# Kernel optimization log

Hardware: AMD Instinct MI355X
Metric: run time of the kernel (lower is better)

## Reference

```python
import jax, jax.numpy as jnp
import numpy as np

N_NODES = 100000
N_EDGES = 1600000
IN_C = 64
HID_C = 2 * IN_C  # 128
OUT_C = 64


def setup_inputs() -> dict:
    key = jax.random.key(0)
    k1, k2, k3, k4 = jax.random.split(key, 4)
    x = jax.random.normal(k1, (N_NODES, IN_C), dtype=jnp.float32)
    edge_index = jax.random.randint(k2, (2, N_EDGES), 0, N_NODES, dtype=jnp.int64)
    # Glorot-ish scaled weights
    W3 = jax.random.normal(k3, (IN_C, HID_C), dtype=jnp.float32) / np.sqrt(IN_C)
    b3 = jnp.zeros((HID_C,), dtype=jnp.float32)
    W4 = jax.random.normal(k4, (HID_C, OUT_C), dtype=jnp.float32) / np.sqrt(HID_C)
    b4 = jnp.zeros((OUT_C,), dtype=jnp.float32)
    return {"x": x, "edge_index": edge_index, "W3": W3, "b3": b3, "W4": W4, "b4": b4}


def _gcn_conv(x, src, dst, norm, W, b, n_nodes):
    # linear transform first (PyG GCNConv: lin then propagate), then
    # degree-normalized gather-scatter aggregation, then bias.
    h = x @ W                              # [N, C_out]
    msg = h[src] * norm[:, None]           # [E+N, C_out] gathered messages
    out = jax.ops.segment_sum(msg, dst, num_segments=n_nodes)
    return out + b


def reference(x, edge_index, W3, b3, W4, b4):
    n_nodes = x.shape[0]
    # add self-loops (PyG GCNConv default add_self_loops=True)
    loops = jnp.arange(n_nodes, dtype=edge_index.dtype)
    src = jnp.concatenate([edge_index[0], loops])  # [E+N]
    dst = jnp.concatenate([edge_index[1], loops])  # [E+N]
    # symmetric normalization: deg over target column incl. self-loops
    deg = jax.ops.segment_sum(jnp.ones(dst.shape, dtype=x.dtype), dst, num_segments=n_nodes)
    dinv = jnp.where(deg > 0, jax.lax.rsqrt(deg), jnp.zeros_like(deg))
    norm = dinv[src] * dinv[dst]                   # [E+N]
    h = jax.nn.relu(_gcn_conv(x, src, dst, norm, W3, b3, n_nodes))
    return _gcn_conv(h, src, dst, norm, W4, b4, n_nodes)
```

## Files before the change

kernel.cpp:

```cpp
#include <hip/hip_runtime.h>
#include <hip/hip_bf16.h>
#include <hip/hip_fp16.h>


constexpr int IN_C  = 64;
constexpr int HID_C = 128;
constexpr int OUT_C = 64;
constexpr int BSHIFT = 9;
constexpr int BW     = 1 << BSHIFT;
constexpr int TILE   = 4096;
constexpr int FCAP   = 16384;

typedef _Float16 f16x8 __attribute__((ext_vector_type(8)));
typedef float    f32x4 __attribute__((ext_vector_type(4)));

union FragU { uint4 u; f16x8 h; _Float16 q[8]; };

__device__ __forceinline__ f32x4 mfma16(f16x8 a, f16x8 b, f32x4 c) {
    return __builtin_amdgcn_mfma_f32_16x16x32_f16(a, b, c, 0, 0, 0);
}

__device__ __forceinline__ float2 up2(unsigned u) {
    __half2 h = *reinterpret_cast<__half2*>(&u);
    return __half22float2(h);
}
__device__ __forceinline__ unsigned pk2(float a, float b) {
    __half2 h = __float22half2_rn(make_float2(a, b));
    return *reinterpret_cast<unsigned*>(&h);
}

__global__ __launch_bounds__(256) void zero_small_kernel(int* __restrict__ p, int m)
{
    int i = blockIdx.x * 256 + threadIdx.x;
    if (i < m) p[i] = 0;
}

__global__ __launch_bounds__(256) void wfrag_kernel(
    const float* __restrict__ W3, const float* __restrict__ W4,
    uint4* __restrict__ w3f, uint4* __restrict__ w4f)
{
    const int idx = blockIdx.x * 256 + threadIdx.x;
    const int l = idx & 63, cl = l & 15, ch = l >> 4;
    if (idx < 2048) {
        const int fi = idx >> 6;
        const int h = fi & 1, s = (fi >> 1) & 1, c = fi >> 2;
        const int k0 = s * 32 + ch * 8, col = c * 16 + cl;
        FragU f;
        #pragma unroll
        for (int i = 0; i < 8; ++i) {
            float x = W3[(k0 + i) * HID_C + col];
            _Float16 hi = (_Float16)x;
            f.q[i] = h ? (_Float16)(x - (float)hi) : hi;
        }
        w3f[fi * 64 + l] = f.u;
    } else if (idx < 3072) {
        const int fi = (idx - 2048) >> 6;
        const int s = fi & 3, c = fi >> 2;
        const int k0 = s * 32 + ch * 8, col = c * 16 + cl;
        FragU f;
        #pragma unroll
        for (int i = 0; i < 8; ++i)
            f.q[i] = (_Float16)W4[(k0 + i) * OUT_C + col];
        w4f[fi * 64 + l] = f.u;
    }
}

__global__ __launch_bounds__(256) void bhist_kernel(
    const int* __restrict__ dst, int* __restrict__ bcnt, int E, int nbkt)
{
    __shared__ int h[256];
    h[threadIdx.x] = 0;
    __syncthreads();
    const int stride = gridDim.x * 256;
    for (int e = blockIdx.x * 256 + threadIdx.x; e < E; e += stride) {
        int d = __builtin_nontemporal_load(&dst[e]);
        atomicAdd(&h[d >> BSHIFT], 1);
    }
    __syncthreads();
    if (threadIdx.x < nbkt && h[threadIdx.x] != 0)
        atomicAdd(&bcnt[threadIdx.x], h[threadIdx.x]);
}

__global__ __launch_bounds__(256) void bscan_kernel(
    const int* __restrict__ bcnt, int* __restrict__ bbase,
    int* __restrict__ bcur, int nbkt)
{
    __shared__ int s[256];
    int v = (threadIdx.x < nbkt) ? bcnt[threadIdx.x] : 0;
    s[threadIdx.x] = v;
    __syncthreads();
    for (int off = 1; off < 256; off <<= 1) {
        int t = (threadIdx.x >= off) ? s[threadIdx.x - off] : 0;
        __syncthreads();
        s[threadIdx.x] += t;
        __syncthreads();
    }
    if (threadIdx.x < nbkt) {
        int ex = s[threadIdx.x] - v;
        bbase[threadIdx.x] = ex;
        bcur[threadIdx.x]  = ex;
        if (threadIdx.x == nbkt - 1) bbase[nbkt] = s[threadIdx.x];
    }
}

__global__ __launch_bounds__(256) void bin_kernel(
    const int* __restrict__ src, const int* __restrict__ dst,
    int* __restrict__ bcur, unsigned* __restrict__ ebuf, int E, int nbkt)
{
    __shared__ unsigned stageS[TILE];
    __shared__ unsigned char stageB[TILE];
    __shared__ int lcnt[256], lofs[256], lpos[256], gbase[256], s[256];
    const int base = blockIdx.x * TILE;
    const int cnt_mine = min(TILE, E - base);
    const int t = threadIdx.x;
    lcnt[t] = 0;
    __syncthreads();
    unsigned w[16]; int p[16];
    #pragma unroll
    for (int k = 0; k < 16; ++k) {
        int jo = t + k * 256;
        if (jo < cnt_mine) {
            int sv = __builtin_nontemporal_load(&src[base + jo]);
            int dv = __builtin_nontemporal_load(&dst[base + jo]);
            p[k] = dv >> BSHIFT;
            w[k] = ((unsigned)sv << BSHIFT) | (unsigned)(dv & (BW - 1));
            atomicAdd(&lcnt[p[k]], 1);
        } else p[k] = -1;
    }
    __syncthreads();
    int v = lcnt[t];
    s[t] = v;
    __syncthreads();
    for (int off = 1; off < 256; off <<= 1) {
        int u = (t >= off) ? s[t - off] : 0;
        __syncthreads();
        s[t] += u;
        __syncthreads();
    }
    lofs[t] = s[t] - v;
    lpos[t] = s[t] - v;
    if (t < nbkt && v != 0) gbase[t] = atomicAdd(&bcur[t], v);
    __syncthreads();
    #pragma unroll
    for (int k = 0; k < 16; ++k) {
        if (p[k] >= 0) {
            int pos = atomicAdd(&lpos[p[k]], 1);
            stageS[pos] = w[k];
            stageB[pos] = (unsigned char)p[k];
        }
    }
    __syncthreads();
    for (int j = t; j < cnt_mine; j += 256) {
        int b = stageB[j];
        ebuf[gbase[b] + (j - lofs[b])] = stageS[j];
    }
}

__global__ __launch_bounds__(256) void bucket_kernel(
    const unsigned* __restrict__ ebuf, const int* __restrict__ bbase,
    int* __restrict__ row_start, float* __restrict__ dinv,
    int* __restrict__ sorted_src, int n, int E, int nbkt)
{
    __shared__ int lcnt[BW];
    __shared__ int lcur[BW];
    __shared__ int s[256];
    __shared__ int lsrc[FCAP];
    const int b   = blockIdx.x;
    const int lo  = b << BSHIFT;
    const int hi  = min(lo + BW, n);
    const int nn  = hi - lo;
    const int beg = bbase[b], end = bbase[b + 1];
    const int cnt = end - beg;
    const int t   = threadIdx.x;
    for (int i = t; i < nn; i += 256) lcnt[i] = 0;
    __syncthreads();
    for (int j = beg + t; j < end; j += 256)
        atomicAdd(&lcnt[ebuf[j] & (BW - 1)], 1);
    __syncthreads();
    int a0 = (2 * t     < nn) ? lcnt[2 * t]     : 0;
    int a1 = (2 * t + 1 < nn) ? lcnt[2 * t + 1] : 0;
    int tsum = a0 + a1;
    s[t] = tsum;
    __syncthreads();
    for (int off = 1; off < 256; off <<= 1) {
        int v = (t >= off) ? s[t - off] : 0;
        __syncthreads();
        s[t] += v;
        __syncthreads();
    }
    int texcl = s[t] - tsum;
    if (2 * t < nn) {
        lcur[2 * t] = texcl;
        row_start[lo + 2 * t] = beg + texcl;
        dinv[lo + 2 * t] = rsqrtf((float)a0 + 1.0f);
    }
    if (2 * t + 1 < nn) {
        lcur[2 * t + 1] = texcl + a0;
        row_start[lo + 2 * t + 1] = beg + texcl + a0;
        dinv[lo + 2 * t + 1] = rsqrtf((float)a1 + 1.0f);
    }
    if (t == 0 && b == nbkt - 1) row_start[n] = E;
    __syncthreads();
    if (cnt <= FCAP) {
        for (int j = beg + t; j < end; j += 256) {
            unsigned w = ebuf[j];
            int pos = atomicAdd(&lcur[w & (BW - 1)], 1);
            lsrc[pos] = (int)(w >> BSHIFT);
        }
        __syncthreads();
        for (int j = t; j < cnt; j += 256)
            sorted_src[beg + j] = lsrc[j];
    } else {
        for (int j = beg + t; j < end; j += 256) {
            unsigned w = ebuf[j];
            int pos = atomicAdd(&lcur[w & (BW - 1)], 1);
            sorted_src[beg + pos] = (int)(w >> BSHIFT);
        }
    }
}

__global__ __launch_bounds__(256) void cvt_scaled_kernel(
    const float2* __restrict__ in, const float* __restrict__ dinv,
    unsigned* __restrict__ outw, int nw)
{
    int i = blockIdx.x * 256 + threadIdx.x;
    if (i < nw) {
        float2 v = in[i];
        float dv = dinv[i >> 5];
        outw[i] = pk2(v.x * dv, v.y * dv);
    }
}

template <bool OUT_F16, bool ADD_BIAS>
__global__ __launch_bounds__(256) void agg_f16_kernel(
    const unsigned* __restrict__ feat, const int* __restrict__ row_start,
    const int* __restrict__ sorted_src, const float* __restrict__ dinv,
    const float* __restrict__ bias, void* __restrict__ outp, int n)
{
    const int g  = threadIdx.x >> 3;
    const int gl = threadIdx.x & 7;
    const int d  = blockIdx.x * 32 + g;
    if (d >= n) return;
    const float di = dinv[d];
    const uint4* f4 = (const uint4*)feat;

    float a0x, a0y, a1x, a1y, a2x, a2y, a3x, a3y;
    {
        uint4 u = f4[(size_t)d * 8 + gl];
        float2 f0 = up2(u.x), f1 = up2(u.y), f2 = up2(u.z), f3 = up2(u.w);
        a0x = f0.x; a0y = f0.y; a1x = f1.x; a1y = f1.y;
        a2x = f2.x; a2y = f2.y; a3x = f3.x; a3y = f3.y;
    }

#define ACC(U) do { \
        float2 f0_ = up2((U).x), f1_ = up2((U).y), f2_ = up2((U).z), f3_ = up2((U).w); \
        a0x += f0_.x; a0y += f0_.y; a1x += f1_.x; a1y += f1_.y; \
        a2x += f2_.x; a2y += f2_.y; a3x += f3_.x; a3y += f3_.y; } while (0)

    const int beg = row_start[d], end = row_start[d + 1];
    const int last = end - 1;
    int i = beg;
    int s0, s1, s2, s3;
    if (i < end) {
        s0 = sorted_src[i];
        s1 = sorted_src[min(i + 1, last)];
        s2 = sorted_src[min(i + 2, last)];
        s3 = sorted_src[min(i + 3, last)];
    }
    while (i < end) {
        uint4 u0 = f4[(size_t)s0 * 8 + gl];
        uint4 u1 = f4[(size_t)s1 * 8 + gl];
        uint4 u2 = f4[(size_t)s2 * 8 + gl];
        uint4 u3 = f4[(size_t)s3 * 8 + gl];
        const int ni = i + 4;
        if (ni < end) {
            s0 = sorted_src[ni];
            s1 = sorted_src[min(ni + 1, last)];
            s2 = sorted_src[min(ni + 2, last)];
            s3 = sorted_src[min(ni + 3, last)];
        }
        const int nb = end - i;
        ACC(u0);
        if (nb > 1) ACC(u1);
        if (nb > 2) ACC(u2);
        if (nb > 3) ACC(u3);
        i = ni;
    }
#undef ACC

    a0x *= di; a0y *= di; a1x *= di; a1y *= di;
    a2x *= di; a2y *= di; a3x *= di; a3y *= di;
    if (ADD_BIAS) {
        const float4 b0 = ((const float4*)bias)[gl * 2];
        const float4 b1 = ((const float4*)bias)[gl * 2 + 1];
        a0x += b0.x; a0y += b0.y; a1x += b0.z; a1y += b0.w;
        a2x += b1.x; a2y += b1.y; a3x += b1.z; a3y += b1.w;
    }
    if (OUT_F16) {
        uint4 o;
        o.x = pk2(a0x, a0y); o.y = pk2(a1x, a1y);
        o.z = pk2(a2x, a2y); o.w = pk2(a3x, a3y);
        ((uint4*)outp)[(size_t)d * 8 + gl] = o;
    } else {
        float4* op = (float4*)outp;
        op[(size_t)d * 16 + gl * 2]     = make_float4(a0x, a0y, a1x, a1y);
        op[(size_t)d * 16 + gl * 2 + 1] = make_float4(a2x, a2y, a3x, a3y);
    }
}

__global__ __launch_bounds__(256) void gemm12_kernel(
    const unsigned* __restrict__ ax, const uint4* __restrict__ w3f,
    const uint4* __restrict__ w4f, const float* __restrict__ b3,
    const float* __restrict__ dinv, unsigned* __restrict__ t, int n)
{
    __shared__ __align__(16) char lds[32768];
    const int l  = threadIdx.x & 63;
    const int wv = threadIdx.x >> 6;
    const int cl = l & 15, ch = l >> 4;
    const int r0 = blockIdx.x * 128 + wv * 32;

    FragU a1[2][2];
    const uint4* ax4 = (const uint4*)ax;
    #pragma unroll
    for (int rt = 0; rt < 2; ++rt)
        #pragma unroll
        for (int s = 0; s < 2; ++s)
            a1[rt][s].u = ax4[(size_t)(r0 + rt * 16 + cl) * 8 + s * 4 + ch];

    float bb[8];
    #pragma unroll
    for (int c = 0; c < 8; ++c) bb[c] = b3[c * 16 + cl];

    const f32x4 z4 = {0.f, 0.f, 0.f, 0.f};
    f32x4 acc1[2][8];
    #pragma unroll
    for (int rt = 0; rt < 2; ++rt)
        #pragma unroll
        for (int c = 0; c < 8; ++c) acc1[rt][c] = z4;

    #pragma unroll
    for (int c = 0; c < 8; ++c) {
        FragU bh0, bl0, bh1, bl1;
        bh0.u = w3f[(c * 4 + 0) * 64 + l];
        bl0.u = w3f[(c * 4 + 1) * 64 + l];
        bh1.u = w3f[(c * 4 + 2) * 64 + l];
        bl1.u = w3f[(c * 4 + 3) * 64 + l];
        #pragma unroll
        for (int rt = 0; rt < 2; ++rt) {
            f32x4 a = acc1[rt][c];
            a = mfma16(a1[rt][0].h, bh0.h, a);
            a = mfma16(a1[rt][0].h, bl0.h, a);
            a = mfma16(a1[rt][1].h, bh1.h, a);
            a = mfma16(a1[rt][1].h, bl1.h, a);
            acc1[rt][c] = a;
        }
    }

    #pragma unroll
    for (int rt = 0; rt < 2; ++rt) {
        const int tb = (wv * 2 + rt) * 4096;
        #pragma unroll
        for (int c = 0; c < 8; ++c)
            #pragma unroll
            for (int i = 0; i < 4; ++i) {
                int row = ch * 4 + i;
                int off = tb + ((row * 256 + (c * 16 + cl) * 2) ^ ((row & 7) << 4));
                *(_Float16*)&lds[off] =
                    (_Float16)fmaxf(acc1[rt][c][i] + bb[c], 0.0f);
            }
    }

    float dv[2][4];
    #pragma unroll
    for (int rt = 0; rt < 2; ++rt)
        #pragma unroll
        for (int i = 0; i < 4; ++i)
            dv[rt][i] = dinv[min(r0 + rt * 16 + ch * 4 + i, n - 1)];

    FragU a2[2][4];
    #pragma unroll
    for (int rt = 0; rt < 2; ++rt) {
        const int tb = (wv * 2 + rt) * 4096;
        #pragma unroll
        for (int s2 = 0; s2 < 4; ++s2) {
            int off = tb + ((cl * 256 + s2 * 64 + ch * 16) ^ ((cl & 7) << 4));
            a2[rt][s2].u = *(const uint4*)&lds[off];
        }
    }

    f32x4 acc2[2][4];
    #pragma unroll
    for (int rt = 0; rt < 2; ++rt)
        #pragma unroll
        for (int c2 = 0; c2 < 4; ++c2) acc2[rt][c2] = z4;

    #pragma unroll
    for (int c2 = 0; c2 < 4; ++c2)
        #pragma unroll
        for (int s2 = 0; s2 < 4; ++s2) {
            FragU b2; b2.u = w4f[(c2 * 4 + s2) * 64 + l];
            acc2[0][c2] = mfma16(a2[0][s2].h, b2.h, acc2[0][c2]);
            acc2[1][c2] = mfma16(a2[1][s2].h, b2.h, acc2[1][c2]);
        }

    _Float16* th = (_Float16*)t;
    #pragma unroll
    for (int rt = 0; rt < 2; ++rt)
        #pragma unroll
        for (int i = 0; i < 4; ++i) {
            int row = r0 + rt * 16 + ch * 4 + i;
            if (row < n) {
                #pragma unroll
                for (int c2 = 0; c2 < 4; ++c2)
                    th[(size_t)row * 64 + c2 * 16 + cl] =
                        (_Float16)(acc2[rt][c2][i] * dv[rt][i]);
            }
        }
}

extern "C" void kernel_launch(void* const* d_in, const int* in_sizes, int n_in,
                              void* d_out, int out_size, void* d_ws, size_t ws_size,
                              hipStream_t stream)
{
    const float* x  = (const float*)d_in[0];
    const int*   ei = (const int*)d_in[1];
    const float* W3 = (const float*)d_in[2];
    const float* b3 = (const float*)d_in[3];
    const float* W4 = (const float*)d_in[4];
    const float* b4 = (const float*)d_in[5];
    float* out = (float*)d_out;

    const int n = in_sizes[0] / IN_C;
    const int E = in_sizes[1] / 2;
    const int* src = ei;
    const int* dst = ei + E;
    const int nbkt = (n + BW - 1) >> BSHIFT;

    const size_t n_pad = ((size_t)n + 256) & ~(size_t)255;

    int*      bcnt      = (int*)d_ws;
    int*      bbase     = bcnt + 256;
    int*      bcur      = bbase + 512;
    int*      row_start = bcur + 256;
    float*    dinv      = (float*)(row_start + n_pad);
    int*      ssrc      = (int*)(dinv + n_pad);
    unsigned* ebuf      = (unsigned*)(ssrc + (((size_t)E + 255) & ~(size_t)255));
    unsigned* xh        = ebuf + (((size_t)E + 255) & ~(size_t)255);
    unsigned* agg_x     = xh + n_pad * 32;
    uint4*    w3f       = (uint4*)(agg_x + n_pad * 32);
    uint4*    w4f       = w3f + 2048;
    unsigned* t         = xh;

    zero_small_kernel<<<1, 256, 0, stream>>>(bcnt, 256);
    wfrag_kernel<<<12, 256, 0, stream>>>(W3, W4, w3f, w4f);
    bhist_kernel<<<256, 256, 0, stream>>>(dst, bcnt, E, nbkt);
    bscan_kernel<<<1, 256, 0, stream>>>(bcnt, bbase, bcur, nbkt);

    bin_kernel<<<(E + TILE - 1) / TILE, 256, 0, stream>>>(src, dst, bcur, ebuf, E, nbkt);
    bucket_kernel<<<nbkt, 256, 0, stream>>>(ebuf, bbase, row_start, dinv, ssrc, n, E, nbkt);

    cvt_scaled_kernel<<<(n * 32 + 255) / 256, 256, 0, stream>>>(
        (const float2*)x, dinv, xh, n * 32);

    agg_f16_kernel<true, false><<<(n + 31) / 32, 256, 0, stream>>>(
        xh, row_start, ssrc, dinv, nullptr, agg_x, n);

    gemm12_kernel<<<(n + 127) / 128, 256, 0, stream>>>(
        agg_x, w3f, w4f, b3, dinv, t, n);

    agg_f16_kernel<false, true><<<(n + 31) / 32, 256, 0, stream>>>(
        t, row_start, ssrc, dinv, b4, out, n);
}
```

Before: 228.4 us.

## Vectorize edge index loads and double-buffer neighbor feature gathers in aggregation

```diff
diff --git a/kernel.cpp b/kernel.cpp
--- a/kernel.cpp
+++ b/kernel.cpp
@@ -13,6 +13,7 @@
 
 typedef _Float16 f16x8 __attribute__((ext_vector_type(8)));
 typedef float    f32x4 __attribute__((ext_vector_type(4)));
+typedef int      i32x4 __attribute__((ext_vector_type(4)));
 
 union FragU { uint4 u; f16x8 h; _Float16 q[8]; };
 
@@ -71,9 +72,19 @@
     __shared__ int h[256];
     h[threadIdx.x] = 0;
     __syncthreads();
+    const int gid = blockIdx.x * 256 + threadIdx.x;
     const int stride = gridDim.x * 256;
-    for (int e = blockIdx.x * 256 + threadIdx.x; e < E; e += stride) {
-        int d = __builtin_nontemporal_load(&dst[e]);
+    const int E4 = E >> 2;
+    const i32x4* d4p = (const i32x4*)dst;
+    for (int e = gid; e < E4; e += stride) {
+        i32x4 d4 = __builtin_nontemporal_load(&d4p[e]);
+        atomicAdd(&h[d4.x >> BSHIFT], 1);
+        atomicAdd(&h[d4.y >> BSHIFT], 1);
+        atomicAdd(&h[d4.z >> BSHIFT], 1);
+        atomicAdd(&h[d4.w >> BSHIFT], 1);
+    }
+    if (gid < (E & 3)) {
+        int d = dst[E4 * 4 + gid];
         atomicAdd(&h[d >> BSHIFT], 1);
     }
     __syncthreads();
@@ -116,16 +127,35 @@
     lcnt[t] = 0;
     __syncthreads();
     unsigned w[16]; int p[16];
-    #pragma unroll
-    for (int k = 0; k < 16; ++k) {
-        int jo = t + k * 256;
-        if (jo < cnt_mine) {
-            int sv = __builtin_nontemporal_load(&src[base + jo]);
-            int dv = __builtin_nontemporal_load(&dst[base + jo]);
-            p[k] = dv >> BSHIFT;
-            w[k] = ((unsigned)sv << BSHIFT) | (unsigned)(dv & (BW - 1));
-            atomicAdd(&lcnt[p[k]], 1);
-        } else p[k] = -1;
+    if (base + TILE <= E) {
+        const i32x4* s4p = (const i32x4*)(src + base);
+        const i32x4* d4p = (const i32x4*)(dst + base);
+        #pragma unroll
+        for (int k4 = 0; k4 < 4; ++k4) {
+            i32x4 s4 = __builtin_nontemporal_load(&s4p[t + k4 * 256]);
+            i32x4 d4 = __builtin_nontemporal_load(&d4p[t + k4 * 256]);
+            #pragma unroll
+            for (int j = 0; j < 4; ++j) {
+                int k = k4 * 4 + j;
+                int sv = (j == 0) ? s4.x : (j == 1) ? s4.y : (j == 2) ? s4.z : s4.w;
+                int dv = (j == 0) ? d4.x : (j == 1) ? d4.y : (j == 2) ? d4.z : d4.w;
+                p[k] = dv >> BSHIFT;
+                w[k] = ((unsigned)sv << BSHIFT) | (unsigned)(dv & (BW - 1));
+                atomicAdd(&lcnt[p[k]], 1);
+            }
+        }
+    } else {
+        #pragma unroll
+        for (int k = 0; k < 16; ++k) {
+            int jo = t + k * 256;
+            if (jo < cnt_mine) {
+                int sv = __builtin_nontemporal_load(&src[base + jo]);
+                int dv = __builtin_nontemporal_load(&dst[base + jo]);
+                p[k] = dv >> BSHIFT;
+                w[k] = ((unsigned)sv << BSHIFT) | (unsigned)(dv & (BW - 1));
+                atomicAdd(&lcnt[p[k]], 1);
+            } else p[k] = -1;
+        }
     }
     __syncthreads();
     int v = lcnt[t];
@@ -256,37 +286,65 @@
         float2 f0_ = up2((U).x), f1_ = up2((U).y), f2_ = up2((U).z), f3_ = up2((U).w); \
         a0x += f0_.x; a0y += f0_.y; a1x += f1_.x; a1y += f1_.y; \
         a2x += f2_.x; a2y += f2_.y; a3x += f3_.x; a3y += f3_.y; } while (0)
+#define LDIDX(v0, v1, v2, v3, at) do { \
+        v0 = __builtin_nontemporal_load(&sorted_src[(at)]); \
+        v1 = __builtin_nontemporal_load(&sorted_src[min((at) + 1, last)]); \
+        v2 = __builtin_nontemporal_load(&sorted_src[min((at) + 2, last)]); \
+        v3 = __builtin_nontemporal_load(&sorted_src[min((at) + 3, last)]); } while (0)
 
     const int beg = row_start[d], end = row_start[d + 1];
     const int last = end - 1;
     int i = beg;
-    int s0, s1, s2, s3;
+    int ia0 = 0, ia1 = 0, ia2 = 0, ia3 = 0;
+    int ib0 = 0, ib1 = 0, ib2 = 0, ib3 = 0;
+    uint4 uA0, uA1, uA2, uA3, uB0, uB1, uB2, uB3;
     if (i < end) {
-        s0 = sorted_src[i];
-        s1 = sorted_src[min(i + 1, last)];
-        s2 = sorted_src[min(i + 2, last)];
-        s3 = sorted_src[min(i + 3, last)];
+        LDIDX(ia0, ia1, ia2, ia3, i);
+        uA0 = f4[(size_t)ia0 * 8 + gl];
+        uA1 = f4[(size_t)ia1 * 8 + gl];
+        uA2 = f4[(size_t)ia2 * 8 + gl];
+        uA3 = f4[(size_t)ia3 * 8 + gl];
+        if (i + 4 < end) LDIDX(ib0, ib1, ib2, ib3, i + 4);
     }
     while (i < end) {
-        uint4 u0 = f4[(size_t)s0 * 8 + gl];
-        uint4 u1 = f4[(size_t)s1 * 8 + gl];
-        uint4 u2 = f4[(size_t)s2 * 8 + gl];
-        uint4 u3 = f4[(size_t)s3 * 8 + gl];
-        const int ni = i + 4;
+        int ni = i + 4;
         if (ni < end) {
-            s0 = sorted_src[ni];
-            s1 = sorted_src[min(ni + 1, last)];
-            s2 = sorted_src[min(ni + 2, last)];
-            s3 = sorted_src[min(ni + 3, last)];
-        }
-        const int nb = end - i;
-        ACC(u0);
-        if (nb > 1) ACC(u1);
-        if (nb > 2) ACC(u2);
-        if (nb > 3) ACC(u3);
+            uB0 = f4[(size_t)ib0 * 8 + gl];
+            uB1 = f4[(size_t)ib1 * 8 + gl];
+            uB2 = f4[(size_t)ib2 * 8 + gl];
+            uB3 = f4[(size_t)ib3 * 8 + gl];
+        }
+        int nn2 = ni + 4;
+        if (nn2 < end) LDIDX(ia0, ia1, ia2, ia3, nn2);
+        {
+            int nb = end - i;
+            ACC(uA0);
+            if (nb > 1) ACC(uA1);
+            if (nb > 2) ACC(uA2);
+            if (nb > 3) ACC(uA3);
+        }
         i = ni;
+        if (i >= end) break;
+        ni = i + 4;
+        if (ni < end) {
+            uA0 = f4[(size_t)ia0 * 8 + gl];
+            uA1 = f4[(size_t)ia1 * 8 + gl];
+            uA2 = f4[(size_t)ia2 * 8 + gl];
+            uA3 = f4[(size_t)ia3 * 8 + gl];
+        }
+        nn2 = ni + 4;
+        if (nn2 < end) LDIDX(ib0, ib1, ib2, ib3, nn2);
+        {
+            int nb = end - i;
+            ACC(uB0);
+            if (nb > 1) ACC(uB1);
+            if (nb > 2) ACC(uB2);
+            if (nb > 3) ACC(uB3);
+        }
+        i = ni;
     }
 #undef ACC
+#undef LDIDX
 
     a0x *= di; a0y *= di; a1x *= di; a1y *= di;
     a2x *= di; a2y *= di; a3x *= di; a3y *= di;
```

After: 229.7 us. Within noise of the previous version (+0.6%).
